# Performance work log

Hardware: AMD Instinct MI355X
Metric: run time of the kernel (lower is better)

Reference implementation:

```python
import jax, jax.numpy as jnp
import numpy as np

NF4 = jnp.array([-1.0, -0.6961928009986877, -0.5250730514526367, -0.39491748809814453,
                 -0.28444138169288635, -0.18477343022823334, -0.09105003625154495, 0.0,
                 0.07958029955625534, 0.16093020141124725, 0.24611230194568634,
                 0.33791524171829224, 0.44070982933044434, 0.5626170039176941,
                 0.7229568362236023, 1.0], dtype=jnp.float32)

IN_FEATURES = 2048
OUT_FEATURES = 8192
BLOCK_SIZE = 64


def setup_inputs() -> dict:
    key = jax.random.key(0)
    k1, k2, k3, k4 = jax.random.split(key, 4)
    n_elems = OUT_FEATURES * IN_FEATURES
    n_blocks = n_elems // BLOCK_SIZE
    x = jax.random.normal(k1, (2, 2048, IN_FEATURES), dtype=jnp.float32)
    q = jax.random.randint(k2, (n_elems,), 0, 16, dtype=jnp.int32)
    scale = jax.random.uniform(k3, (n_blocks,), dtype=jnp.float32)  # absmax >= 0
    bias = jax.random.normal(k4, (OUT_FEATURES,), dtype=jnp.float32)
    return {"x": x, "q": q, "scale": scale, "bias": bias}


def reference(x, q, scale, bias):
    # Dequantize: NF4 table lookup per 4-bit code, per-block absmax scale.
    n_blocks = scale.shape[0]
    codes = q.reshape(n_blocks, BLOCK_SIZE)                  # (n_blocks, 64)
    w = NF4[codes] * scale[:, None]                          # (n_blocks, 64)
    w = w.reshape(OUT_FEATURES, IN_FEATURES)                 # (out, in)
    # F.linear: y = x @ W^T + b
    return jnp.einsum('bsi,oi->bso', x, w) + bias
```

## Files before the change

### kernel.cpp

```cpp
#include <hip/hip_runtime.h>
#include <stdint.h>

#define GM 4096
#define GN 8192
#define GK 2048

typedef float f32x4 __attribute__((ext_vector_type(4)));
typedef __bf16 bf16x8 __attribute__((ext_vector_type(8)));

__device__ __constant__ float NF4_LUT[16] = {
    -1.0f, -0.6961928009986877f, -0.5250730514526367f, -0.39491748809814453f,
    -0.28444138169288635f, -0.18477343022823334f, -0.09105003625154495f, 0.0f,
    0.07958029955625534f, 0.16093020141124725f, 0.24611230194568634f,
    0.33791524171829224f, 0.44070982933044434f, 0.5626170039176941f,
    0.7229568362236023f, 1.0f};

__device__ __forceinline__ unsigned short f32_to_bf16_rne(float f) {
  union { float f; uint32_t u; } v;
  v.f = f;
  uint32_t lsb = (v.u >> 16) & 1u;
  v.u += 0x7fffu + lsb;
  return (unsigned short)(v.u >> 16);
}

__global__ void __launch_bounds__(256) dequant_nf4_kernel(
    const int* __restrict__ q, const float* __restrict__ scale,
    unsigned short* __restrict__ w) {
  __shared__ float lut[16];
  if (threadIdx.x < 16) lut[threadIdx.x] = NF4_LUT[threadIdx.x];
  __syncthreads();
  int t = blockIdx.x * 256 + threadIdx.x;
  const int4* q4 = reinterpret_cast<const int4*>(q);
  int4 c0 = q4[2 * t];
  int4 c1 = q4[2 * t + 1];
  float s = scale[t >> 3];
  int codes[8] = {c0.x, c0.y, c0.z, c0.w, c1.x, c1.y, c1.z, c1.w};
  union { unsigned short u[8]; int4 v; } r;
#pragma unroll
  for (int j = 0; j < 8; ++j)
    r.u[j] = f32_to_bf16_rne(lut[codes[j] & 15] * s);
  reinterpret_cast<int4*>(w)[t] = r.v;
}

__global__ void __launch_bounds__(256) cvt_f32_bf16_kernel(
    const float* __restrict__ x, unsigned short* __restrict__ xb) {
  int t = blockIdx.x * 256 + threadIdx.x;
  const float4* x4 = reinterpret_cast<const float4*>(x);
  float4 a = x4[2 * t];
  float4 b = x4[2 * t + 1];
  union { unsigned short u[8]; int4 v; } r;
  r.u[0] = f32_to_bf16_rne(a.x); r.u[1] = f32_to_bf16_rne(a.y);
  r.u[2] = f32_to_bf16_rne(a.z); r.u[3] = f32_to_bf16_rne(a.w);
  r.u[4] = f32_to_bf16_rne(b.x); r.u[5] = f32_to_bf16_rne(b.y);
  r.u[6] = f32_to_bf16_rne(b.z); r.u[7] = f32_to_bf16_rne(b.w);
  reinterpret_cast<int4*>(xb)[t] = r.v;
}

#define AS1(p) ((const __attribute__((address_space(1))) void*)(p))
#define AS3(p) ((__attribute__((address_space(3))) void*)(p))
#define VM6() asm volatile("s_waitcnt vmcnt(6)" ::: "memory")
#define VM0() asm volatile("s_waitcnt vmcnt(0)" ::: "memory")
#define LGKM0() do { asm volatile("s_waitcnt lgkmcnt(0)" ::: "memory"); \
                     __builtin_amdgcn_sched_barrier(0); } while (0)
#define BAR() __builtin_amdgcn_s_barrier()

__global__ void __launch_bounds__(512, 2) gemm_8phase_kernel(
    const unsigned short* __restrict__ A,
    const unsigned short* __restrict__ B,
    const float* __restrict__ bias, float* __restrict__ C) {
  constexpr int BK = 64, NT = GK / BK;
  __shared__ __align__(16) unsigned short As[2 * 256 * 64];
  __shared__ __align__(16) unsigned short Bs[2 * 256 * 64];

  int bid = blockIdx.x;
  int swz = (bid & 7) * 64 + (bid >> 3);
  int brow = (swz >> 5) * 256;
  int bcol = (swz & 31) * 256;

  int tid = threadIdx.x;
  int lane = tid & 63;
  int wave = tid >> 6;
  int wr = wave >> 2;
  int wc = wave & 3;
  int fr = lane & 15;
  int slot = lane >> 4;
  int swc = (slot << 4) ^ ((fr & 7) << 4);

  const unsigned short* Abase = A + (size_t)brow * GK;
  const unsigned short* Bbase = B + (size_t)bcol * GK;

  int arow = (wr * 64 + fr) * 128;
  int brw = (wc * 32 + fr) * 128;

  f32x4 acc[8][4] = {};
  bf16x8 af[4][2], bf[4][2];

  auto ldA = [&](int buf, int qm, int m, int kk) -> bf16x8 {
    int off = buf * 32768 + qm * 16384 + m * 2048 + arow + (swc ^ (kk << 6));
    return *reinterpret_cast<const bf16x8*>((const char*)As + off);
  };
  auto ldB = [&](int buf, int qn, int n, int kk) -> bf16x8 {
    int off = buf * 32768 + qn * 16384 + n * 2048 + brw + (swc ^ (kk << 6));
    return *reinterpret_cast<const bf16x8*>((const char*)Bs + off);
  };
  auto stageA = [&](int tt) {
    (void)tt;
  };
  auto stage = [&](const unsigned short* gtile, unsigned short* lds, int buf,
                   int h, int kt) {
#pragma unroll
    for (int i = 0; i < 2; ++i) {
      int L = h * 16384 + i * 8192 + tid * 16;
      int s = L ^ (((L >> 7) & 7) << 4);
      __builtin_amdgcn_global_load_lds(
          AS1(gtile + (size_t)(s >> 7) * GK + kt + ((s & 127) >> 1)),
          AS3((char*)lds + buf * 32768 + L), 16, 0, 0);
    }
  };

  stage(Abase, As, 0, 0, 0);
  stage(Bbase, Bs, 0, 0, 0);
  stage(Bbase, Bs, 0, 1, 0);
  stage(Abase, As, 0, 1, 0);
  stage(Abase, As, 1, 0, BK);
  stage(Bbase, Bs, 1, 0, BK);
  VM6();
  BAR();

  for (int tt = 0; tt < NT; ++tt) {
    int buf = tt & 1;
    int nbuf = buf ^ 1;
#pragma unroll
    for (int m = 0; m < 4; ++m) {
#pragma unroll
      for (int kk = 0; kk < 2; ++kk) af[m][kk] = ldA(buf, 0, m, kk);
    }
#pragma unroll
    for (int n = 0; n < 2; ++n) {
#pragma unroll
      for (int kk = 0; kk < 2; ++kk) bf[n][kk] = ldB(buf, 0, n, kk);
    }
    if (tt + 1 < NT) stage(Bbase, Bs, nbuf, 1, (tt + 1) * BK);
    BAR();
    LGKM0();
    __builtin_amdgcn_s_setprio(1);
#pragma unroll
    for (int m = 0; m < 4; ++m)
#pragma unroll
      for (int n = 0; n < 2; ++n)
#pragma unroll
        for (int kk = 0; kk < 2; ++kk)
          acc[m][n] = __builtin_amdgcn_mfma_f32_16x16x32_bf16(
              af[m][kk], bf[n][kk], acc[m][n], 0, 0, 0);
    __builtin_amdgcn_s_setprio(0);
    BAR();
#pragma unroll
    for (int n = 2; n < 4; ++n) {
#pragma unroll
      for (int kk = 0; kk < 2; ++kk) bf[n][kk] = ldB(buf, 1, n - 2, kk);
    }
    if (tt + 1 < NT) stage(Abase, As, nbuf, 1, (tt + 1) * BK);
    if (tt >= NT - 2) { VM0(); } else { VM6(); }
    BAR();
    LGKM0();
    __builtin_amdgcn_s_setprio(1);
#pragma unroll
    for (int m = 0; m < 4; ++m)
#pragma unroll
      for (int n = 2; n < 4; ++n)
#pragma unroll
        for (int kk = 0; kk < 2; ++kk)
          acc[m][n] = __builtin_amdgcn_mfma_f32_16x16x32_bf16(
              af[m][kk], bf[n][kk], acc[m][n], 0, 0, 0);
    __builtin_amdgcn_s_setprio(0);
    BAR();
#pragma unroll
    for (int m = 0; m < 4; ++m) {
#pragma unroll
      for (int kk = 0; kk < 2; ++kk) af[m][kk] = ldA(buf, 1, m, kk);
    }
    if (tt + 2 < NT) stage(Abase, As, buf, 0, (tt + 2) * BK);
    BAR();
    LGKM0();
    __builtin_amdgcn_s_setprio(1);
#pragma unroll
    for (int m = 0; m < 4; ++m)
#pragma unroll
      for (int n = 0; n < 2; ++n)
#pragma unroll
        for (int kk = 0; kk < 2; ++kk)
          acc[4 + m][n] = __builtin_amdgcn_mfma_f32_16x16x32_bf16(
              af[m][kk], bf[n][kk], acc[4 + m][n], 0, 0, 0);
    __builtin_amdgcn_s_setprio(0);
    BAR();
    if (tt + 2 < NT) stage(Bbase, Bs, buf, 0, (tt + 2) * BK);
    if (tt + 1 >= NT - 2) { VM0(); } else { VM6(); }
    BAR();
    __builtin_amdgcn_s_setprio(1);
#pragma unroll
    for (int m = 0; m < 4; ++m)
#pragma unroll
      for (int n = 2; n < 4; ++n)
#pragma unroll
        for (int kk = 0; kk < 2; ++kk)
          acc[4 + m][n] = __builtin_amdgcn_mfma_f32_16x16x32_bf16(
              af[m][kk], bf[n][kk], acc[4 + m][n], 0, 0, 0);
    __builtin_amdgcn_s_setprio(0);
    BAR();
  }

  float bv[4];
#pragma unroll
  for (int n = 0; n < 4; ++n)
    bv[n] = bias[bcol + (n >> 1) * 128 + wc * 32 + (n & 1) * 16 + fr];
#pragma unroll
  for (int m = 0; m < 8; ++m) {
    int grow0 = brow + (m >> 2) * 128 + wr * 64 + (m & 3) * 16 + slot * 4;
#pragma unroll
    for (int n = 0; n < 4; ++n) {
      int gcol = bcol + (n >> 1) * 128 + wc * 32 + (n & 1) * 16 + fr;
#pragma unroll
      for (int r = 0; r < 4; ++r)
        C[(size_t)(grow0 + r) * GN + gcol] = acc[m][n][r] + bv[n];
    }
  }
}

__global__ void __launch_bounds__(256) fallback_kernel(
    const float* __restrict__ x, const int* __restrict__ q,
    const float* __restrict__ scale, const float* __restrict__ bias,
    float* __restrict__ out) {
  __shared__ float wrow[GK];
  int n = blockIdx.x;
  for (int k = threadIdx.x; k < GK; k += 256) {
    size_t idx = (size_t)n * GK + k;
    wrow[k] = NF4_LUT[q[idx] & 15] * scale[idx >> 6];
  }
  __syncthreads();
  int m = blockIdx.y * 256 + threadIdx.x;
  const float* xr = x + (size_t)m * GK;
  float acc = 0.f;
  for (int k = 0; k < GK; ++k) acc += xr[k] * wrow[k];
  out[(size_t)m * GN + n] = acc + bias[n];
}

extern "C" void kernel_launch(void* const* d_in, const int* in_sizes, int n_in,
                              void* d_out, int out_size, void* d_ws, size_t ws_size,
                              hipStream_t stream) {
  const float* x = (const float*)d_in[0];
  const int* q = (const int*)d_in[1];
  const float* scale = (const float*)d_in[2];
  const float* bias = (const float*)d_in[3];
  float* out = (float*)d_out;

  const size_t wbytes = (size_t)GN * GK * 2;
  const size_t xbytes = (size_t)GM * GK * 2;

  if (ws_size >= wbytes + xbytes) {
    unsigned short* wq = (unsigned short*)d_ws;
    unsigned short* xb = (unsigned short*)((char*)d_ws + wbytes);
    dequant_nf4_kernel<<<(GN * GK / 8) / 256, 256, 0, stream>>>(q, scale, wq);
    cvt_f32_bf16_kernel<<<(GM * GK / 8) / 256, 256, 0, stream>>>(x, xb);
    gemm_8phase_kernel<<<dim3((GM / 256) * (GN / 256)), 512, 0, stream>>>(
        xb, wq, bias, out);
  } else {
    fallback_kernel<<<dim3(GN, GM / 256), 256, 0, stream>>>(x, q, scale, bias, out);
  }
}
```

Measured before the change: 167.7 us.

## Restructure GEMM main loop into two-tile unrolled ping-pong with register double buffering

Rewrites the 8-phase GEMM main loop to process two K-tiles per iteration with separate register sets for A/B fragments. LDS reads for the next quadrant or tile are issued before the current MFMA block. The explicit lgkmcnt waits and sched barriers are dropped in favour of compiler memory fences around barriers, and the global-to-LDS staging order changes. The aim is to hide LDS read latency behind MFMAs and cut per-phase wait stalls. The cost is much higher VGPR pressure, which could cause spills or lower occupancy under launch_bounds(512,2). Tail handling clamps to NT-1 and re-stages redundant tiles.

```diff
diff --git a/kernel.cpp b/kernel.cpp
--- a/kernel.cpp
+++ b/kernel.cpp
@@ -59,10 +59,8 @@
 #define AS1(p) ((const __attribute__((address_space(1))) void*)(p))
 #define AS3(p) ((__attribute__((address_space(3))) void*)(p))
 #define VM6() asm volatile("s_waitcnt vmcnt(6)" ::: "memory")
-#define VM0() asm volatile("s_waitcnt vmcnt(0)" ::: "memory")
-#define LGKM0() do { asm volatile("s_waitcnt lgkmcnt(0)" ::: "memory"); \
-                     __builtin_amdgcn_sched_barrier(0); } while (0)
-#define BAR() __builtin_amdgcn_s_barrier()
+#define FENCE() asm volatile("" ::: "memory")
+#define BAR() do { FENCE(); __builtin_amdgcn_s_barrier(); FENCE(); } while (0)
 
 __global__ void __launch_bounds__(512, 2) gemm_8phase_kernel(
     const unsigned short* __restrict__ A,
@@ -93,7 +91,7 @@
   int brw = (wc * 32 + fr) * 128;
 
   f32x4 acc[8][4] = {};
-  bf16x8 af[4][2], bf[4][2];
+  bf16x8 a0[2][4][2], a1[2][4][2], b0[2][2][2], b1[2][2][2];
 
   auto ldA = [&](int buf, int qm, int m, int kk) -> bf16x8 {
     int off = buf * 32768 + qm * 16384 + m * 2048 + arow + (swc ^ (kk << 6));
@@ -102,9 +100,6 @@
   auto ldB = [&](int buf, int qn, int n, int kk) -> bf16x8 {
     int off = buf * 32768 + qn * 16384 + n * 2048 + brw + (swc ^ (kk << 6));
     return *reinterpret_cast<const bf16x8*>((const char*)Bs + off);
-  };
-  auto stageA = [&](int tt) {
-    (void)tt;
   };
   auto stage = [&](const unsigned short* gtile, unsigned short* lds, int buf,
                    int h, int kt) {
@@ -117,96 +112,126 @@
           AS3((char*)lds + buf * 32768 + L), 16, 0, 0);
     }
   };
+  auto RD_A1 = [&](int p) {
+#pragma unroll
+    for (int m = 0; m < 4; ++m)
+#pragma unroll
+      for (int kk = 0; kk < 2; ++kk) a1[p][m][kk] = ldA(p, 1, m, kk);
+  };
+  auto RD_B1 = [&](int p) {
+#pragma unroll
+    for (int n = 0; n < 2; ++n)
+#pragma unroll
+      for (int kk = 0; kk < 2; ++kk) b1[p][n][kk] = ldB(p, 1, n, kk);
+  };
+  auto RD_A0B0 = [&](int p) {
+#pragma unroll
+    for (int m = 0; m < 4; ++m)
+#pragma unroll
+      for (int kk = 0; kk < 2; ++kk) a0[p][m][kk] = ldA(p, 0, m, kk);
+#pragma unroll
+    for (int n = 0; n < 2; ++n)
+#pragma unroll
+      for (int kk = 0; kk < 2; ++kk) b0[p][n][kk] = ldB(p, 0, n, kk);
+  };
+  auto Q1 = [&](int p) {
+    __builtin_amdgcn_s_setprio(1);
+#pragma unroll
+    for (int m = 0; m < 4; ++m)
+#pragma unroll
+      for (int n = 0; n < 2; ++n)
+#pragma unroll
+        for (int kk = 0; kk < 2; ++kk)
+          acc[m][n] = __builtin_amdgcn_mfma_f32_16x16x32_bf16(
+              a0[p][m][kk], b0[p][n][kk], acc[m][n], 0, 0, 0);
+    __builtin_amdgcn_s_setprio(0);
+  };
+  auto Q2 = [&](int p) {
+    __builtin_amdgcn_s_setprio(1);
+#pragma unroll
+    for (int m = 0; m < 4; ++m)
+#pragma unroll
+      for (int n = 0; n < 2; ++n)
+#pragma unroll
+        for (int kk = 0; kk < 2; ++kk)
+          acc[4 + m][n] = __builtin_amdgcn_mfma_f32_16x16x32_bf16(
+              a1[p][m][kk], b0[p][n][kk], acc[4 + m][n], 0, 0, 0);
+    __builtin_amdgcn_s_setprio(0);
+  };
+  auto Q3 = [&](int p) {
+    __builtin_amdgcn_s_setprio(1);
+#pragma unroll
+    for (int m = 0; m < 4; ++m)
+#pragma unroll
+      for (int n = 0; n < 2; ++n)
+#pragma unroll
+        for (int kk = 0; kk < 2; ++kk)
+          acc[4 + m][2 + n] = __builtin_amdgcn_mfma_f32_16x16x32_bf16(
+              a1[p][m][kk], b1[p][n][kk], acc[4 + m][2 + n], 0, 0, 0);
+    __builtin_amdgcn_s_setprio(0);
+  };
+  auto Q4 = [&](int p) {
+    __builtin_amdgcn_s_setprio(1);
+#pragma unroll
+    for (int m = 0; m < 4; ++m)
+#pragma unroll
+      for (int n = 0; n < 2; ++n)
+#pragma unroll
+        for (int kk = 0; kk < 2; ++kk)
+          acc[m][2 + n] = __builtin_amdgcn_mfma_f32_16x16x32_bf16(
+              a0[p][m][kk], b1[p][n][kk], acc[m][2 + n], 0, 0, 0);
+    __builtin_amdgcn_s_setprio(0);
+  };
 
   stage(Abase, As, 0, 0, 0);
   stage(Bbase, Bs, 0, 0, 0);
+  stage(Abase, As, 0, 1, 0);
   stage(Bbase, Bs, 0, 1, 0);
-  stage(Abase, As, 0, 1, 0);
   stage(Abase, As, 1, 0, BK);
   stage(Bbase, Bs, 1, 0, BK);
+  stage(Abase, As, 1, 1, BK);
   VM6();
   BAR();
-
-  for (int tt = 0; tt < NT; ++tt) {
-    int buf = tt & 1;
-    int nbuf = buf ^ 1;
-#pragma unroll
-    for (int m = 0; m < 4; ++m) {
-#pragma unroll
-      for (int kk = 0; kk < 2; ++kk) af[m][kk] = ldA(buf, 0, m, kk);
-    }
-#pragma unroll
-    for (int n = 0; n < 2; ++n) {
-#pragma unroll
-      for (int kk = 0; kk < 2; ++kk) bf[n][kk] = ldB(buf, 0, n, kk);
-    }
-    if (tt + 1 < NT) stage(Bbase, Bs, nbuf, 1, (tt + 1) * BK);
-    BAR();
-    LGKM0();
-    __builtin_amdgcn_s_setprio(1);
-#pragma unroll
-    for (int m = 0; m < 4; ++m)
-#pragma unroll
-      for (int n = 0; n < 2; ++n)
-#pragma unroll
-        for (int kk = 0; kk < 2; ++kk)
-          acc[m][n] = __builtin_amdgcn_mfma_f32_16x16x32_bf16(
-              af[m][kk], bf[n][kk], acc[m][n], 0, 0, 0);
-    __builtin_amdgcn_s_setprio(0);
-    BAR();
-#pragma unroll
-    for (int n = 2; n < 4; ++n) {
-#pragma unroll
-      for (int kk = 0; kk < 2; ++kk) bf[n][kk] = ldB(buf, 1, n - 2, kk);
-    }
-    if (tt + 1 < NT) stage(Abase, As, nbuf, 1, (tt + 1) * BK);
-    if (tt >= NT - 2) { VM0(); } else { VM6(); }
-    BAR();
-    LGKM0();
-    __builtin_amdgcn_s_setprio(1);
-#pragma unroll
-    for (int m = 0; m < 4; ++m)
-#pragma unroll
-      for (int n = 2; n < 4; ++n)
-#pragma unroll
-        for (int kk = 0; kk < 2; ++kk)
-          acc[m][n] = __builtin_amdgcn_mfma_f32_16x16x32_bf16(
-              af[m][kk], bf[n][kk], acc[m][n], 0, 0, 0);
-    __builtin_amdgcn_s_setprio(0);
-    BAR();
-#pragma unroll
-    for (int m = 0; m < 4; ++m) {
-#pragma unroll
-      for (int kk = 0; kk < 2; ++kk) af[m][kk] = ldA(buf, 1, m, kk);
-    }
-    if (tt + 2 < NT) stage(Abase, As, buf, 0, (tt + 2) * BK);
-    BAR();
-    LGKM0();
-    __builtin_amdgcn_s_setprio(1);
-#pragma unroll
-    for (int m = 0; m < 4; ++m)
-#pragma unroll
-      for (int n = 0; n < 2; ++n)
-#pragma unroll
-        for (int kk = 0; kk < 2; ++kk)
-          acc[4 + m][n] = __builtin_amdgcn_mfma_f32_16x16x32_bf16(
-              af[m][kk], bf[n][kk], acc[4 + m][n], 0, 0, 0);
-    __builtin_amdgcn_s_setprio(0);
-    BAR();
-    if (tt + 2 < NT) stage(Bbase, Bs, buf, 0, (tt + 2) * BK);
-    if (tt + 1 >= NT - 2) { VM0(); } else { VM6(); }
-    BAR();
-    __builtin_amdgcn_s_setprio(1);
-#pragma unroll
-    for (int m = 0; m < 4; ++m)
-#pragma unroll
-      for (int n = 2; n < 4; ++n)
-#pragma unroll
-        for (int kk = 0; kk < 2; ++kk)
-          acc[4 + m][n] = __builtin_amdgcn_mfma_f32_16x16x32_bf16(
-              af[m][kk], bf[n][kk], acc[4 + m][n], 0, 0, 0);
-    __builtin_amdgcn_s_setprio(0);
-    BAR();
+  RD_A0B0(0);
+
+#pragma unroll 1
+  for (int j = 0; j < NT / 2; ++j) {
+    int t1 = 2 * j + 1;
+    int t2 = (2 * j + 2 < NT) ? 2 * j + 2 : NT - 1;
+    int t3 = (2 * j + 3 < NT) ? 2 * j + 3 : NT - 1;
+    int kt1 = t1 * BK, kt2 = t2 * BK, kt3 = t3 * BK;
+    RD_A1(0);
+    stage(Bbase, Bs, 1, 1, kt1);
+    BAR();
+    Q1(0);
+    RD_B1(0);
+    BAR();
+    Q2(0);
+    stage(Abase, As, 0, 0, kt2);
+    stage(Bbase, Bs, 0, 0, kt2);
+    BAR();
+    Q3(0);
+    stage(Abase, As, 0, 1, kt2);
+    VM6();
+    BAR();
+    RD_A0B0(1);
+    Q4(0);
+    RD_A1(1);
+    stage(Bbase, Bs, 0, 1, kt2);
+    BAR();
+    Q1(1);
+    RD_B1(1);
+    BAR();
+    Q2(1);
+    stage(Abase, As, 1, 0, kt3);
+    stage(Bbase, Bs, 1, 0, kt3);
+    BAR();
+    Q3(1);
+    stage(Abase, As, 1, 1, kt3);
+    VM6();
+    BAR();
+    RD_A0B0(0);
+    Q4(1);
   }
 
   float bv[4];
```

After: 155.7 us. 7.2% less time.
